# Optimization experiments

Hardware: AMD Instinct MI355X
Metric: run time of the kernel (lower is better)

Reference implementation:

```python
import jax, jax.numpy as jnp
import numpy as np

N = 100_000      # nodes
E = 1_600_000    # edges
EL = 200_000     # labeled edge pairs
NODE_DIM, HID = 32, 256
H2, H4 = HID // 2, HID // 4  # 128, 64


def _lin(k, fan_in, fan_out):
    kw, kb = jax.random.split(k)
    bound = 1.0 / np.sqrt(fan_in)
    W = jax.random.uniform(kw, (fan_in, fan_out), jnp.float32, -bound, bound)
    b = jax.random.uniform(kb, (fan_out,), jnp.float32, -bound, bound)
    return W, b


def setup_inputs() -> dict:
    key = jax.random.key(0)
    ks = jax.random.split(key, 12)
    x = jax.random.normal(ks[0], (N, NODE_DIM), jnp.float32)
    edge_index = jax.random.randint(ks[1], (2, E), 0, N, jnp.int64)
    edge_label_index = jax.random.randint(ks[2], (2, EL), 0, N, jnp.int64)
    enc_w1, enc_b1 = _lin(ks[3], NODE_DIM, HID)
    enc_w2, enc_b2 = _lin(ks[4], HID, H2)
    conv_w0, conv_b0 = _lin(ks[5], H2, H4)
    conv_w1, conv_b1 = _lin(ks[6], H4, H4)
    conv_w2, conv_b2 = _lin(ks[7], H4, H4)
    ep_w1, ep_b1 = _lin(ks[8], 2 * H4, H2)
    ep_w2, ep_b2 = _lin(ks[9], H2, H4)
    ep_w3, ep_b3 = _lin(ks[10], H4, 1)
    return dict(x=x, edge_index=edge_index, edge_label_index=edge_label_index,
                enc_w1=enc_w1, enc_b1=enc_b1, enc_w2=enc_w2, enc_b2=enc_b2,
                conv_w0=conv_w0, conv_b0=conv_b0, conv_w1=conv_w1, conv_b1=conv_b1,
                conv_w2=conv_w2, conv_b2=conv_b2,
                ep_w1=ep_w1, ep_b1=ep_b1, ep_w2=ep_w2, ep_b2=ep_b2, ep_w3=ep_w3, ep_b3=ep_b3)


def reference(x, edge_index, edge_label_index,
              enc_w1, enc_b1, enc_w2, enc_b2,
              conv_w0, conv_b0, conv_w1, conv_b1, conv_w2, conv_b2,
              ep_w1, ep_b1, ep_w2, ep_b2, ep_w3, ep_b3):
    # node encoder (dropout = identity in eval)
    h = jax.nn.relu(x @ enc_w1 + enc_b1)
    h = jax.nn.relu(h @ enc_w2 + enc_b2)           # [N, 128]

    # GCN normalization with self-loops (PyG gcn_norm, edge_weight=1)
    loops = jnp.arange(N, dtype=edge_index.dtype)
    src = jnp.concatenate([edge_index[0], loops])   # [E+N]
    dst = jnp.concatenate([edge_index[1], loops])
    deg = jax.ops.segment_sum(jnp.ones(E + N, jnp.float32), dst, num_segments=N)
    dinv = jnp.where(deg > 0, jax.lax.rsqrt(jnp.maximum(deg, 1.0)), 0.0)
    norm = (dinv[src] * dinv[dst])[:, None]          # [E+N, 1]

    def gcn(h, W, b):
        xw = h @ W                                   # transform first (PyG)
        agg = jax.ops.segment_sum(xw[src] * norm, dst, num_segments=N)
        return agg + b

    for W, b in ((conv_w0, conv_b0), (conv_w1, conv_b1), (conv_w2, conv_b2)):
        h_new = jax.nn.relu(gcn(h, W, b))
        h = h + h_new if h.shape == h_new.shape else h_new
        # self.dropout -> identity in eval

    # edge predictor on labeled pairs
    ef = jnp.concatenate([h[edge_label_index[0]], h[edge_label_index[1]]], axis=1)  # [EL, 128]
    e = jax.nn.relu(ef @ ep_w1 + ep_b1)
    e = jax.nn.relu(e @ ep_w2 + ep_b2)
    e = jax.nn.sigmoid(e @ ep_w3 + ep_b3)
    return e.squeeze(-1)                             # [EL]
```

## Files before the change

### kernel.cpp

```cpp
#include <hip/hip_runtime.h>
#include <math.h>


#define N_NODES 100000
#define N_EDGES 1600000
#define N_EL    200000

#define KBUCK   98
#define WSHIFT  10
#define WMASK   1023
#define BCAP    128
#define BSTRIDE 24576
#define PART_NB 512
#define CHUNK   3125
#define LCAP    20480

typedef __attribute__((ext_vector_type(8))) short short8_t;
typedef __attribute__((ext_vector_type(4))) float f32x4;

__device__ __forceinline__ unsigned short f2bf(float f) {
    unsigned u = __float_as_uint(f);
    unsigned r = u + 0x7FFFu + ((u >> 16) & 1u);
    return (unsigned short)(r >> 16);
}

__device__ __forceinline__ float2 up16(unsigned u) {
    union { unsigned v; _Float16 h[2]; } c; c.v = u;
    return make_float2((float)c.h[0], (float)c.h[1]);
}

template<int KTOT, int NTOT>
__device__ __forceinline__ void wprep_one(const float* __restrict__ W, unsigned short* __restrict__ Wp, int flat) {
    if (flat >= KTOT * NTOT) return;
    int j = flat & 7, lane = (flat >> 3) & 63, kstep = (flat >> 9) & 1;
    int rest = flat >> 10;
    int ntile = rest % (NTOT / 16), chunk = rest / (NTOT / 16);
    int k = chunk * 64 + kstep * 32 + (lane >> 4) * 8 + j;
    int n = ntile * 16 + (lane & 15);
    Wp[flat] = f2bf(W[(size_t)k * NTOT + n]);
}

__device__ __forceinline__ void wprep32_one(const float* __restrict__ W, unsigned short* __restrict__ Wp, int flat) {
    if (flat >= 32 * 256) return;
    int j = flat & 7, lane = (flat >> 3) & 63, ntile = flat >> 9;
    int k = (lane >> 4) * 8 + j;
    int n = ntile * 16 + (lane & 15);
    Wp[flat] = f2bf(W[(size_t)k * 256 + n]);
}

__global__ __launch_bounds__(256) void fill_part(const int* __restrict__ ei,
                                                 int* __restrict__ btail, int* __restrict__ bscr,
    const float* w2, const float* w0, const float* w1, const float* wpp2, const float* w1e,
    const float* wc1, const float* wc2,
    unsigned short* p2, unsigned short* p0, unsigned short* p1, unsigned short* pp2,
    unsigned short* p1e, unsigned short* pc1, unsigned short* pc2)
{
    __shared__ int lbuf[KBUCK][BCAP];
    __shared__ int lcnt[KBUCK];
    __shared__ int offs[KBUCK + 1];
    __shared__ int gbase[KBUCK];
    int t = threadIdx.x;

    if (blockIdx.x >= PART_NB) {
        int blk = blockIdx.x - PART_NB;
        if      (blk < 128) wprep_one<256, 128>(w2,  p2,  blk * 256 + t);
        else if (blk < 160) wprep_one<128,  64>(w0,  p0,  (blk - 128) * 256 + t);
        else if (blk < 224) wprep_one<128, 128>(w1,  p1,  (blk - 160) * 256 + t);
        else if (blk < 256) wprep_one<128,  64>(wpp2, pp2, (blk - 224) * 256 + t);
        else if (blk < 288) wprep32_one(w1e, p1e, (blk - 256) * 256 + t);
        else if (blk < 304) wprep_one< 64,  64>(wc1, pc1, (blk - 288) * 256 + t);
        else                wprep_one< 64,  64>(wc2, pc2, (blk - 304) * 256 + t);
        return;
    }

    for (int i = t; i < KBUCK; i += 256) lcnt[i] = 0;
    __syncthreads();

    int e0   = blockIdx.x * CHUNK;
    int eend = e0 + CHUNK; if (eend > N_EDGES) eend = N_EDGES;
    for (int e = e0 + t; e < eend; e += 256) {
        int s = __builtin_nontemporal_load(ei + e);
        int d = __builtin_nontemporal_load(ei + N_EDGES + e);
        int b = d >> WSHIFT;
        int entry = ((d & WMASK) << 17) | s;
        int pos = atomicAdd(&lcnt[b], 1);
        if (pos < BCAP) lbuf[b][pos] = entry;
        else {
            int p = atomicAdd(&btail[b], 1);
            bscr[b * BSTRIDE + p] = entry;
        }
    }
    __syncthreads();

    if (t < KBUCK) {
        int c = lcnt[t]; if (c > BCAP) c = BCAP;
        lcnt[t] = c;
        gbase[t] = atomicAdd(&btail[t], c);
    }
    __syncthreads();
    if (t == 0) {
        offs[0] = 0;
        for (int b = 0; b < KBUCK; ++b) offs[b + 1] = offs[b] + lcnt[b];
    }
    __syncthreads();

    int T = offs[KBUCK];
    for (int i = t; i < T; i += 256) {
        int loB = 0, hiB = KBUCK;
        while (hiB - loB > 1) { int mid = (loB + hiB) >> 1; if (offs[mid] <= i) loB = mid; else hiB = mid; }
        int j = i - offs[loB];
        bscr[loB * BSTRIDE + gbase[loB] + j] = lbuf[loB][j];
    }
}

__global__ __launch_bounds__(1024) void fill_place(const int* __restrict__ btail,
                                                   const int* __restrict__ bscr,
                                                   int* __restrict__ row_ptr, float* __restrict__ dinv,
                                                   int* __restrict__ col) {
    __shared__ int ssm[128];
    __shared__ int lcnt[1024];
    __shared__ int lpre[1024];
    __shared__ int lbuf[LCAP];
    int b = blockIdx.x, t = threadIdx.x;

    if (t < 128) ssm[t] = (t < KBUCK) ? btail[t] : 0;
    lcnt[t] = 0;
    __syncthreads();
    for (int s = 1; s < 128; s <<= 1) {
        int a = 0;
        if (t < 128 && t >= s) a = ssm[t - s];
        __syncthreads();
        if (t < 128) ssm[t] += a;
        __syncthreads();
    }
    int segstart = (b == 0) ? 0 : ssm[b - 1];
    int n = btail[b];
    const int* src = bscr + b * BSTRIDE;
    for (int i = t; i < n; i += 1024)
        atomicAdd(&lcnt[src[i] >> 17], 1);
    __syncthreads();

    int c = lcnt[t];
    lpre[t] = c; __syncthreads();
    for (int s = 1; s < 1024; s <<= 1) {
        int a = (t >= s) ? lpre[t - s] : 0;
        __syncthreads();
        lpre[t] += a;
        __syncthreads();
    }
    int excl = lpre[t] - c;

    int v = (b << WSHIFT) + t;
    if (v < N_NODES) {
        row_ptr[v] = segstart + excl;
        dinv[v] = rsqrtf((float)(c + 1));
    }
    if (b == KBUCK - 1 && t == 0) row_ptr[N_NODES] = N_EDGES;
    lcnt[t] = excl;
    __syncthreads();

    if (n <= LCAP) {
        for (int i = t; i < n; i += 1024) {
            int e = src[i];
            int pos = atomicAdd(&lcnt[e >> 17], 1);
            lbuf[pos] = e & 0x1FFFF;
        }
        __syncthreads();
        for (int i = t; i < n; i += 1024)
            col[segstart + i] = lbuf[i];
    } else {
        for (int i = t; i < n; i += 1024) {
            int e = src[i];
            int pos = atomicAdd(&lcnt[e >> 17], 1);
            col[segstart + pos] = e & 0x1FFFF;
        }
    }
}

__global__ __launch_bounds__(256, 3) void mfma_encfull(
    const float* __restrict__ x,
    const unsigned short* __restrict__ Wp1, const float* __restrict__ b1,
    const unsigned short* __restrict__ Wp2, const float* __restrict__ b2,
    const unsigned short* __restrict__ Wp0, const float* __restrict__ dinv,
    _Float16* __restrict__ yout, int M)
{
    __shared__ __align__(16) unsigned short smem[25088];
    unsigned short (*As)[40]   = (unsigned short(*)[40])smem;
    unsigned short* Wls1       = smem + 2560;
    unsigned short (*H1)[264]  = (unsigned short(*)[264])smem;
    unsigned short (*H128)[136]= (unsigned short(*)[136])smem;
    unsigned short* Wls2       = smem + 16896;
    unsigned short* W0s        = smem + 16896;

    int t = threadIdx.x, wave = t >> 6, lane = t & 63;
    int m0 = blockIdx.x * 64;
    int cb = lane & 15, rq = lane >> 4;

    {
        int row = t >> 2, seg = t & 3;
        int gr = m0 + row;
        float4 a = make_float4(0.f, 0.f, 0.f, 0.f), b = a;
        if (gr < M) {
            a = *(const float4*)&x[(size_t)gr * 32 + seg * 8];
            b = *(const float4*)&x[(size_t)gr * 32 + seg * 8 + 4];
        }
        unsigned short tmp[8] = { f2bf(a.x), f2bf(a.y), f2bf(a.z), f2bf(a.w),
                                  f2bf(b.x), f2bf(b.y), f2bf(b.z), f2bf(b.w) };
        *(uint4*)&As[row][seg * 8] = *(uint4*)tmp;
    }
    #pragma unroll
    for (int j = 0; j < 4; ++j)
        ((uint4*)Wls1)[t + j * 256] = ((const uint4*)Wp1)[t + j * 256];
    __syncthreads();

    short8_t af1 = *(const short8_t*)&As[wave * 16 + cb][rq * 8];
    f32x4 acc[16];
    #pragma unroll
    for (int nt = 0; nt < 16; ++nt) {
        short8_t bf = *(const short8_t*)&Wls1[(nt * 64 + lane) * 8];
        acc[nt] = __builtin_amdgcn_mfma_f32_16x16x32_bf16(af1, bf, (f32x4){0.f, 0.f, 0.f, 0.f}, 0, 0, 0);
    }
    __syncthreads();

    #pragma unroll
    for (int nt = 0; nt < 16; ++nt) {
        int col = nt * 16 + cb;
        float bv = b1[col];
        #pragma unroll
        for (int r = 0; r < 4; ++r)
            H1[wave * 16 + rq * 4 + r][col] = f2bf(fmaxf(acc[nt][r] + bv, 0.f));
    }

    f32x4 acc2[8];
    #pragma unroll
    for (int nt = 0; nt < 8; ++nt) acc2[nt] = (f32x4){0.f, 0.f, 0.f, 0.f};
    for (int ch = 0; ch < 4; ++ch) {
        #pragma unroll
        for (int j = 0; j < 4; ++j)
            ((uint4*)Wls2)[t + j * 256] = ((const uint4*)(Wp2 + (size_t)ch * 8192))[t + j * 256];
        __syncthreads();
        #pragma unroll
        for (int ks = 0; ks < 2; ++ks) {
            short8_t af = *(const short8_t*)&H1[wave * 16 + cb][ch * 64 + ks * 32 + rq * 8];
            #pragma unroll
            for (int nt = 0; nt < 8; ++nt) {
                short8_t bf = *(const short8_t*)&Wls2[((nt * 2 + ks) * 64 + lane) * 8];
                acc2[nt] = __builtin_amdgcn_mfma_f32_16x16x32_bf16(af, bf, acc2[nt], 0, 0, 0);
            }
        }
        __syncthreads();
    }

    #pragma unroll
    for (int nt = 0; nt < 8; ++nt) {
        int col = nt * 16 + cb;
        float bv = b2[col];
        #pragma unroll
        for (int r = 0; r < 4; ++r)
            H128[wave * 16 + rq * 4 + r][col] = f2bf(fmaxf(acc2[nt][r] + bv, 0.f));
    }
    ((uint4*)W0s)[t]       = ((const uint4*)Wp0)[t];
    ((uint4*)W0s)[t + 256] = ((const uint4*)Wp0)[t + 256];
    __syncthreads();

    f32x4 acc3[4];
    #pragma unroll
    for (int nt = 0; nt < 4; ++nt) acc3[nt] = (f32x4){0.f, 0.f, 0.f, 0.f};
    #pragma unroll
    for (int ch = 0; ch < 2; ++ch) {
        #pragma unroll
        for (int ks = 0; ks < 2; ++ks) {
            short8_t af = *(const short8_t*)&H128[wave * 16 + cb][ch * 64 + ks * 32 + rq * 8];
            #pragma unroll
            for (int nt = 0; nt < 4; ++nt) {
                short8_t bf = *(const short8_t*)&W0s[(((ch * 4 + nt) * 2 + ks) * 64 + lane) * 8];
                acc3[nt] = __builtin_amdgcn_mfma_f32_16x16x32_bf16(af, bf, acc3[nt], 0, 0, 0);
            }
        }
    }

    #pragma unroll
    for (int nt = 0; nt < 4; ++nt) {
        int col = nt * 16 + cb;
        #pragma unroll
        for (int r = 0; r < 4; ++r) {
            int gr = m0 + wave * 16 + rq * 4 + r;
            if (gr < M) yout[(size_t)gr * 64 + col] = (_Float16)(acc3[nt][r] * dinv[gr]);
        }
    }
}

template<bool RESIDUAL>
__device__ __forceinline__ void aggcv_body(
    const uint4* __restrict__ y4, const int* __restrict__ row_ptr, const int* __restrict__ col,
    const float* __restrict__ dinv, const float* __restrict__ bias,
    const unsigned short* __restrict__ Wp,
    float* __restrict__ h,
    _Float16* __restrict__ yout)
{
    __shared__ __align__(16) unsigned short Ws[4096];
    __shared__ __align__(16) unsigned short Hs[32][72];
    __shared__ float Dv[32];

    int t = threadIdx.x;
    ((uint4*)Ws)[t]       = ((const uint4*)Wp)[t];
    ((uint4*)Ws)[t + 256] = ((const uint4*)Wp)[t + 256];

    int n  = t >> 3;
    int sl = t & 7;
    int v  = blockIdx.x * 32 + n;

    uint4 a = y4[(size_t)v * 8 + sl];
    float2 p0 = up16(a.x), p1 = up16(a.y), p2 = up16(a.z), p3 = up16(a.w);
    float s0 = p0.x, s1 = p0.y, s2 = p1.x, s3 = p1.y;
    float s4 = p2.x, s5 = p2.y, s6 = p3.x, s7 = p3.y;

    int s = row_ptr[v], e = row_ptr[v + 1];
    int i = s;
    for (; i + 3 < e; i += 4) {
        int u0 = col[i], u1 = col[i + 1], u2 = col[i + 2], u3 = col[i + 3];
        uint4 f0 = y4[(size_t)u0 * 8 + sl];
        uint4 f1 = y4[(size_t)u1 * 8 + sl];
        uint4 f2 = y4[(size_t)u2 * 8 + sl];
        uint4 f3 = y4[(size_t)u3 * 8 + sl];
        float2 g;
        g = up16(f0.x); s0 += g.x; s1 += g.y;  g = up16(f0.y); s2 += g.x; s3 += g.y;
        g = up16(f0.z); s4 += g.x; s5 += g.y;  g = up16(f0.w); s6 += g.x; s7 += g.y;
        g = up16(f1.x); s0 += g.x; s1 += g.y;  g = up16(f1.y); s2 += g.x; s3 += g.y;
        g = up16(f1.z); s4 += g.x; s5 += g.y;  g = up16(f1.w); s6 += g.x; s7 += g.y;
        g = up16(f2.x); s0 += g.x; s1 += g.y;  g = up16(f2.y); s2 += g.x; s3 += g.y;
        g = up16(f2.z); s4 += g.x; s5 += g.y;  g = up16(f2.w); s6 += g.x; s7 += g.y;
        g = up16(f3.x); s0 += g.x; s1 += g.y;  g = up16(f3.y); s2 += g.x; s3 += g.y;
        g = up16(f3.z); s4 += g.x; s5 += g.y;  g = up16(f3.w); s6 += g.x; s7 += g.y;
    }
    for (; i < e; ++i) {
        uint4 f = y4[(size_t)col[i] * 8 + sl];
        float2 g;
        g = up16(f.x); s0 += g.x; s1 += g.y;  g = up16(f.y); s2 += g.x; s3 += g.y;
        g = up16(f.z); s4 += g.x; s5 += g.y;  g = up16(f.w); s6 += g.x; s7 += g.y;
    }

    float dv = dinv[v];
    float4 ba = *(const float4*)&bias[sl * 8];
    float4 bb = *(const float4*)&bias[sl * 8 + 4];
    float v0 = fmaxf(dv * s0 + ba.x, 0.f), v1 = fmaxf(dv * s1 + ba.y, 0.f);
    float v2 = fmaxf(dv * s2 + ba.z, 0.f), v3 = fmaxf(dv * s3 + ba.w, 0.f);
    float v4 = fmaxf(dv * s4 + bb.x, 0.f), v5 = fmaxf(dv * s5 + bb.y, 0.f);
    float v6 = fmaxf(dv * s6 + bb.z, 0.f), v7 = fmaxf(dv * s7 + bb.w, 0.f);
    if (RESIDUAL) {
        float4 h0 = *(const float4*)&h[(size_t)v * 64 + sl * 8];
        float4 h1 = *(const float4*)&h[(size_t)v * 64 + sl * 8 + 4];
        v0 += h0.x; v1 += h0.y; v2 += h0.z; v3 += h0.w;
        v4 += h1.x; v5 += h1.y; v6 += h1.z; v7 += h1.w;
    }
    *(float4*)&h[(size_t)v * 64 + sl * 8]     = make_float4(v0, v1, v2, v3);
    *(float4*)&h[(size_t)v * 64 + sl * 8 + 4] = make_float4(v4, v5, v6, v7);
    union { unsigned short us[8]; uint4 u; } hb;
    hb.us[0] = f2bf(v0); hb.us[1] = f2bf(v1); hb.us[2] = f2bf(v2); hb.us[3] = f2bf(v3);
    hb.us[4] = f2bf(v4); hb.us[5] = f2bf(v5); hb.us[6] = f2bf(v6); hb.us[7] = f2bf(v7);
    *(uint4*)&Hs[n][sl * 8] = hb.u;
    if (sl == 0) Dv[n] = dv;
    __syncthreads();

    int wave = t >> 6, lane = t & 63;
    int rt   = wave & 1;
    int ct0  = (wave >> 1) * 2;
    f32x4 acc0 = (f32x4){0.f, 0.f, 0.f, 0.f}, acc1 = acc0;
    #pragma unroll
    for (int ks = 0; ks < 2; ++ks) {
        short8_t af = *(const short8_t*)&Hs[rt * 16 + (lane & 15)][ks * 32 + (lane >> 4) * 8];
        short8_t b0 = *(const short8_t*)&Ws[((ct0 * 2 + ks) * 64 + lane) * 8];
        short8_t b1 = *(const short8_t*)&Ws[(((ct0 + 1) * 2 + ks) * 64 + lane) * 8];
        acc0 = __builtin_amdgcn_mfma_f32_16x16x32_bf16(af, b0, acc0, 0, 0, 0);
        acc1 = __builtin_amdgcn_mfma_f32_16x16x32_bf16(af, b1, acc1, 0, 0, 0);
    }
    int cb = lane & 15, rq = lane >> 4;
    #pragma unroll
    for (int r = 0; r < 4; ++r) {
        int row = rt * 16 + rq * 4 + r;
        float dv2 = Dv[row];
        size_t go = (size_t)(blockIdx.x * 32 + row) * 64;
        yout[go + ct0 * 16 + cb]       = (_Float16)(acc0[r] * dv2);
        yout[go + (ct0 + 1) * 16 + cb] = (_Float16)(acc1[r] * dv2);
    }
}

__global__ __launch_bounds__(256, 6) void aggcv0_kernel(
    const uint4* y, const int* rp, const int* col, const float* dinv, const float* b,
    const unsigned short* Wp, float* h, _Float16* yout) {
    aggcv_body<false>(y, rp, col, dinv, b, Wp, h, yout);
}
__global__ __launch_bounds__(256, 6) void aggcv1_kernel(
    const uint4* y, const int* rp, const int* col, const float* dinv, const float* b,
    const unsigned short* Wp, float* h, _Float16* yout) {
    aggcv_body<true>(y, rp, col, dinv, b, Wp, h, yout);
}

__global__ __launch_bounds__(256) void agg2_kernel(
    const uint4* __restrict__ y4, const int* __restrict__ row_ptr, const int* __restrict__ col,
    const float* __restrict__ dinv, const float* __restrict__ bias,
    const float* __restrict__ hprev, uint4* __restrict__ hb4)
{
    int v  = blockIdx.x * 32 + (threadIdx.x >> 3);
    int sl = threadIdx.x & 7;
    if (v >= N_NODES) return;

    uint4 a = y4[(size_t)v * 8 + sl];
    float2 p0 = up16(a.x), p1 = up16(a.y), p2 = up16(a.z), p3 = up16(a.w);
    float s0 = p0.x, s1 = p0.y, s2 = p1.x, s3 = p1.y;
    float s4 = p2.x, s5 = p2.y, s6 = p3.x, s7 = p3.y;

    int s = row_ptr[v], e = row_ptr[v + 1];
    int i = s;
    for (; i + 3 < e; i += 4) {
        int u0 = col[i], u1 = col[i + 1], u2 = col[i + 2], u3 = col[i + 3];
        uint4 f0 = y4[(size_t)u0 * 8 + sl];
        uint4 f1 = y4[(size_t)u1 * 8 + sl];
        uint4 f2 = y4[(size_t)u2 * 8 + sl];
        uint4 f3 = y4[(size_t)u3 * 8 + sl];
        float2 g;
        g = up16(f0.x); s0 += g.x; s1 += g.y;  g = up16(f0.y); s2 += g.x; s3 += g.y;
        g = up16(f0.z); s4 += g.x; s5 += g.y;  g = up16(f0.w); s6 += g.x; s7 += g.y;
        g = up16(f1.x); s0 += g.x; s1 += g.y;  g = up16(f1.y); s2 += g.x; s3 += g.y;
        g = up16(f1.z); s4 += g.x; s5 += g.y;  g = up16(f1.w); s6 += g.x; s7 += g.y;
        g = up16(f2.x); s0 += g.x; s1 += g.y;  g = up16(f2.y); s2 += g.x; s3 += g.y;
        g = up16(f2.z); s4 += g.x; s5 += g.y;  g = up16(f2.w); s6 += g.x; s7 += g.y;
        g = up16(f3.x); s0 += g.x; s1 += g.y;  g = up16(f3.y); s2 += g.x; s3 += g.y;
        g = up16(f3.z); s4 += g.x; s5 += g.y;  g = up16(f3.w); s6 += g.x; s7 += g.y;
    }
    for (; i < e; ++i) {
        uint4 f = y4[(size_t)col[i] * 8 + sl];
        float2 g;
        g = up16(f.x); s0 += g.x; s1 += g.y;  g = up16(f.y); s2 += g.x; s3 += g.y;
        g = up16(f.z); s4 += g.x; s5 += g.y;  g = up16(f.w); s6 += g.x; s7 += g.y;
    }

    float dv = dinv[v];
    float4 ba = *(const float4*)&bias[sl * 8];
    float4 bb = *(const float4*)&bias[sl * 8 + 4];
    float v0 = fmaxf(dv * s0 + ba.x, 0.f), v1 = fmaxf(dv * s1 + ba.y, 0.f);
    float v2 = fmaxf(dv * s2 + ba.z, 0.f), v3 = fmaxf(dv * s3 + ba.w, 0.f);
    float v4 = fmaxf(dv * s4 + bb.x, 0.f), v5 = fmaxf(dv * s5 + bb.y, 0.f);
    float v6 = fmaxf(dv * s6 + bb.z, 0.f), v7 = fmaxf(dv * s7 + bb.w, 0.f);
    {
        float4 h0 = *(const float4*)&hprev[(size_t)v * 64 + sl * 8];
        float4 h1 = *(const float4*)&hprev[(size_t)v * 64 + sl * 8 + 4];
        v0 += h0.x; v1 += h0.y; v2 += h0.z; v3 += h0.w;
        v4 += h1.x; v5 += h1.y; v6 += h1.z; v7 += h1.w;
    }
    uint4 p;
    p.x = (unsigned)f2bf(v0) | ((unsigned)f2bf(v1) << 16);
    p.y = (unsigned)f2bf(v2) | ((unsigned)f2bf(v3) << 16);
    p.z = (unsigned)f2bf(v4) | ((unsigned)f2bf(v5) << 16);
    p.w = (unsigned)f2bf(v6) | ((unsigned)f2bf(v7) << 16);
    hb4[(size_t)v * 8 + sl] = p;
}

__global__ __launch_bounds__(256, 4) void mfma_ep12(
    const unsigned short* __restrict__ A, const int* __restrict__ gidx,
    const unsigned short* __restrict__ Wp1, const float* __restrict__ b1,
    const unsigned short* __restrict__ Wp2, const float* __restrict__ b2,
    const float* __restrict__ w3, const float* __restrict__ b3,
    float* __restrict__ out, int M)
{
    __shared__ __align__(16) unsigned short smem[12800];
    unsigned short (*As)[72] = (unsigned short(*)[72])smem;
    unsigned short* Wls = smem + 4608;

    int t = threadIdx.x, wave = t >> 6, lane = t & 63;
    int m0 = blockIdx.x * 64;
    int cb = lane & 15, rq = lane >> 4;

    f32x4 acc[8];
    #pragma unroll
    for (int nt = 0; nt < 8; ++nt) acc[nt] = (f32x4){0.f, 0.f, 0.f, 0.f};

    for (int ch = 0; ch < 2; ++ch) {
        #pragma unroll
        for (int j = 0; j < 2; ++j) {
            int idx = t + j * 256;
            int row = idx >> 3, seg = idx & 7;
            int gr = m0 + row;
            uint4 v = make_uint4(0u, 0u, 0u, 0u);
            if (gr < M) {
                int node = (ch == 0) ? gidx[gr] : gidx[N_EL + gr];
                v = *(const uint4*)(A + (size_t)node * 64 + seg * 8);
            }
            *(uint4*)&As[row][seg * 8] = v;
        }
        #pragma unroll
        for (int j = 0; j < 4; ++j) {
            int idx = t + j * 256;
            ((uint4*)Wls)[idx] = ((const uint4*)(Wp1 + (size_t)ch * 8192))[idx];
        }
        __syncthreads();

        #pragma unroll
        for (int ks = 0; ks < 2; ++ks) {
            short8_t af = *(const short8_t*)&As[wave * 16 + cb][ks * 32 + rq * 8];
            #pragma unroll
            for (int nt = 0; nt < 8; ++nt) {
                short8_t bf = *(const short8_t*)&Wls[((nt * 2 + ks) * 64 + lane) * 8];
                acc[nt] = __builtin_amdgcn_mfma_f32_16x16x32_bf16(af, bf, acc[nt], 0, 0, 0);
            }
        }
        __syncthreads();
    }

    unsigned short (*E1)[136] = (unsigned short(*)[136])smem;
    unsigned short* W2s = smem + 8704;
    #pragma unroll
    for (int nt = 0; nt < 8; ++nt) {
        int col = nt * 16 + cb;
        float bv = b1[col];
        #pragma unroll
        for (int r = 0; r < 4; ++r) {
            int row = wave * 16 + rq * 4 + r;
            E1[row][col] = f2bf(fmaxf(acc[nt][r] + bv, 0.f));
        }
    }
    ((uint4*)W2s)[t]       = ((const uint4*)Wp2)[t];
    ((uint4*)W2s)[t + 256] = ((const uint4*)Wp2)[t + 256];
    __syncthreads();

    f32x4 acc2[4];
    #pragma unroll
    for (int nt = 0; nt < 4; ++nt) acc2[nt] = (f32x4){0.f, 0.f, 0.f, 0.f};
    #pragma unroll
    for (int ch = 0; ch < 2; ++ch) {
        #pragma unroll
        for (int ks = 0; ks < 2; ++ks) {
            short8_t af = *(const short8_t*)&E1[wave * 16 + cb][ch * 64 + ks * 32 + rq * 8];
            #pragma unroll
            for (int nt = 0; nt < 4; ++nt) {
                short8_t bf = *(const short8_t*)&W2s[(((ch * 4 + nt) * 2 + ks) * 64 + lane) * 8];
                acc2[nt] = __builtin_amdgcn_mfma_f32_16x16x32_bf16(af, bf, acc2[nt], 0, 0, 0);
            }
        }
    }

    float s0 = 0.f, s1 = 0.f, s2 = 0.f, s3 = 0.f;
    #pragma unroll
    for (int nt = 0; nt < 4; ++nt) {
        int col = nt * 16 + cb;
        float bv = b2[col], wv = w3[col];
        s0 += fmaxf(acc2[nt][0] + bv, 0.f) * wv;
        s1 += fmaxf(acc2[nt][1] + bv, 0.f) * wv;
        s2 += fmaxf(acc2[nt][2] + bv, 0.f) * wv;
        s3 += fmaxf(acc2[nt][3] + bv, 0.f) * wv;
    }
    #pragma unroll
    for (int off = 1; off < 16; off <<= 1) {
        s0 += __shfl_xor(s0, off);
        s1 += __shfl_xor(s1, off);
        s2 += __shfl_xor(s2, off);
        s3 += __shfl_xor(s3, off);
    }
    if (cb == 0) {
        int gr = m0 + wave * 16 + rq * 4;
        if (gr + 3 < M) {
            float bb = b3[0];
            float4 o;
            o.x = 1.f / (1.f + expf(-(s0 + bb)));
            o.y = 1.f / (1.f + expf(-(s1 + bb)));
            o.z = 1.f / (1.f + expf(-(s2 + bb)));
            o.w = 1.f / (1.f + expf(-(s3 + bb)));
            *(float4*)&out[gr] = o;
        }
    }
}

extern "C" void kernel_launch(void* const* d_in, const int* in_sizes, int n_in,
                              void* d_out, int out_size, void* d_ws, size_t ws_size,
                              hipStream_t stream) {
    const float* x       = (const float*)d_in[0];
    const int*   ei      = (const int*)d_in[1];
    const int*   eli     = (const int*)d_in[2];
    const float* enc_w1  = (const float*)d_in[3];
    const float* enc_b1  = (const float*)d_in[4];
    const float* enc_w2  = (const float*)d_in[5];
    const float* enc_b2  = (const float*)d_in[6];
    const float* conv_w0 = (const float*)d_in[7];
    const float* conv_b0 = (const float*)d_in[8];
    const float* conv_w1 = (const float*)d_in[9];
    const float* conv_b1 = (const float*)d_in[10];
    const float* conv_w2 = (const float*)d_in[11];
    const float* conv_b2 = (const float*)d_in[12];
    const float* ep_w1   = (const float*)d_in[13];
    const float* ep_b1   = (const float*)d_in[14];
    const float* ep_w2   = (const float*)d_in[15];
    const float* ep_b2   = (const float*)d_in[16];
    const float* ep_w3   = (const float*)d_in[17];
    const float* ep_b3   = (const float*)d_in[18];
    float* out = (float*)d_out;

    float* fws = (float*)d_ws;
    _Float16* yb         = (_Float16*)fws;
    float* h64           = fws + 3200000;
    unsigned short* h64b = (unsigned short*)(fws + 9600000);
    int*   col     = (int*)(fws + 12800000);
    int*   row_ptr = col + 1600000;
    float* dinvp   = (float*)(row_ptr + 100032);
    unsigned short* w2p = (unsigned short*)(dinvp + 100000);
    unsigned short* w0p = w2p + 32768;
    unsigned short* w1p = w0p + 8192;
    unsigned short* wp2 = w1p + 16384;
    unsigned short* w1e = wp2 + 8192;
    unsigned short* wc1p = w1e + 8192;
    unsigned short* wc2p = wc1p + 4096;
    int*   btail   = (int*)(wc2p + 4096);
    int*   bscr    = btail + 128;

    _Float16* yb2 = (_Float16*)h64b;

    hipMemsetAsync(btail, 0, 128 * sizeof(int), stream);
    fill_part<<<PART_NB + 320, 256, 0, stream>>>(ei, btail, bscr,
        enc_w2, conv_w0, ep_w1, ep_w2, enc_w1, conv_w1, conv_w2,
        w2p, w0p, w1p, wp2, w1e, wc1p, wc2p);
    fill_place<<<KBUCK, 1024, 0, stream>>>(btail, bscr, row_ptr, dinvp, col);

    const int GBN = (N_NODES + 63) / 64;
    const int GBE = N_EL / 64;
    const int GBA = N_NODES / 32;

    mfma_encfull<<<GBN, 256, 0, stream>>>(x, w1e, enc_b1, w2p, enc_b2, w0p, dinvp, yb, N_NODES);

    aggcv0_kernel<<<GBA, 256, 0, stream>>>((const uint4*)yb, row_ptr, col, dinvp, conv_b0,
                                           wc1p, h64, yb2);
    aggcv1_kernel<<<GBA, 256, 0, stream>>>((const uint4*)yb2, row_ptr, col, dinvp, conv_b1,
                                           wc2p, h64, yb);
    agg2_kernel<<<GBA, 256, 0, stream>>>((const uint4*)yb, row_ptr, col, dinvp, conv_b2,
                                         h64, (uint4*)h64b);

    mfma_ep12<<<GBE, 256, 0, stream>>>(h64b, eli, w1p, ep_b1, wp2, ep_b2, ep_w3, ep_b3, out, N_EL);
}
```

Baseline: 295.8 us.

## Double CSR-build bucket count with smaller blocks, unroll neighbor gather by eight

The CSR construction now uses 196 destination buckets of 512 nodes each, handled by 512-thread fill_place blocks instead of 98 buckets of 1024. This spreads the placement work over more CUs with smaller shared-memory footprints. The aggregation kernels now issue eight neighbor-row gathers per iteration before accumulating, which raises memory-level parallelism at some register cost. The local-buffer and per-bucket capacities shrink along with the bucket size, so a skewed bucket is more likely to fall back to the direct-to-global path.

Measured after the change: 294.7 us. No clear change (-0.4%).

```diff
diff --git a/kernel.cpp b/kernel.cpp
--- a/kernel.cpp
+++ b/kernel.cpp
@@ -6,14 +6,14 @@
 #define N_EDGES 1600000
 #define N_EL    200000
 
-#define KBUCK   98
-#define WSHIFT  10
-#define WMASK   1023
-#define BCAP    128
-#define BSTRIDE 24576
+#define KBUCK   196
+#define WSHIFT  9
+#define WMASK   511
+#define BCAP    64
+#define BSTRIDE 12288
 #define PART_NB 512
 #define CHUNK   3125
-#define LCAP    20480
+#define LCAP    10240
 
 typedef __attribute__((ext_vector_type(8))) short short8_t;
 typedef __attribute__((ext_vector_type(4))) float f32x4;
@@ -113,36 +113,36 @@
     }
 }
 
-__global__ __launch_bounds__(1024) void fill_place(const int* __restrict__ btail,
-                                                   const int* __restrict__ bscr,
-                                                   int* __restrict__ row_ptr, float* __restrict__ dinv,
-                                                   int* __restrict__ col) {
-    __shared__ int ssm[128];
-    __shared__ int lcnt[1024];
-    __shared__ int lpre[1024];
+__global__ __launch_bounds__(512) void fill_place(const int* __restrict__ btail,
+                                                  const int* __restrict__ bscr,
+                                                  int* __restrict__ row_ptr, float* __restrict__ dinv,
+                                                  int* __restrict__ col) {
+    __shared__ int ssm[256];
+    __shared__ int lcnt[512];
+    __shared__ int lpre[512];
     __shared__ int lbuf[LCAP];
     int b = blockIdx.x, t = threadIdx.x;
 
-    if (t < 128) ssm[t] = (t < KBUCK) ? btail[t] : 0;
+    if (t < 256) ssm[t] = (t < KBUCK) ? btail[t] : 0;
     lcnt[t] = 0;
     __syncthreads();
-    for (int s = 1; s < 128; s <<= 1) {
+    for (int s = 1; s < 256; s <<= 1) {
         int a = 0;
-        if (t < 128 && t >= s) a = ssm[t - s];
-        __syncthreads();
-        if (t < 128) ssm[t] += a;
+        if (t < 256 && t >= s) a = ssm[t - s];
+        __syncthreads();
+        if (t < 256) ssm[t] += a;
         __syncthreads();
     }
     int segstart = (b == 0) ? 0 : ssm[b - 1];
     int n = btail[b];
     const int* src = bscr + b * BSTRIDE;
-    for (int i = t; i < n; i += 1024)
+    for (int i = t; i < n; i += 512)
         atomicAdd(&lcnt[src[i] >> 17], 1);
     __syncthreads();
 
     int c = lcnt[t];
     lpre[t] = c; __syncthreads();
-    for (int s = 1; s < 1024; s <<= 1) {
+    for (int s = 1; s < 512; s <<= 1) {
         int a = (t >= s) ? lpre[t - s] : 0;
         __syncthreads();
         lpre[t] += a;
@@ -160,16 +160,16 @@
     __syncthreads();
 
     if (n <= LCAP) {
-        for (int i = t; i < n; i += 1024) {
+        for (int i = t; i < n; i += 512) {
             int e = src[i];
             int pos = atomicAdd(&lcnt[e >> 17], 1);
             lbuf[pos] = e & 0x1FFFF;
         }
         __syncthreads();
-        for (int i = t; i < n; i += 1024)
+        for (int i = t; i < n; i += 512)
             col[segstart + i] = lbuf[i];
     } else {
-        for (int i = t; i < n; i += 1024) {
+        for (int i = t; i < n; i += 512) {
             int e = src[i];
             int pos = atomicAdd(&lcnt[e >> 17], 1);
             col[segstart + pos] = e & 0x1FFFF;
@@ -310,43 +310,52 @@
     int sl = t & 7;
     int v  = blockIdx.x * 32 + n;
 
-    uint4 a = y4[(size_t)v * 8 + sl];
-    float2 p0 = up16(a.x), p1 = up16(a.y), p2 = up16(a.z), p3 = up16(a.w);
-    float s0 = p0.x, s1 = p0.y, s2 = p1.x, s3 = p1.y;
-    float s4 = p2.x, s5 = p2.y, s6 = p3.x, s7 = p3.y;
-
-    int s = row_ptr[v], e = row_ptr[v + 1];
-    int i = s;
-    for (; i + 3 < e; i += 4) {
+    float s[8];
+    {
+        uint4 a = y4[(size_t)v * 8 + sl];
+        float2 g;
+        g = up16(a.x); s[0] = g.x; s[1] = g.y;  g = up16(a.y); s[2] = g.x; s[3] = g.y;
+        g = up16(a.z); s[4] = g.x; s[5] = g.y;  g = up16(a.w); s[6] = g.x; s[7] = g.y;
+    }
+    auto accrow = [&](uint4 f) {
+        float2 g;
+        g = up16(f.x); s[0] += g.x; s[1] += g.y;  g = up16(f.y); s[2] += g.x; s[3] += g.y;
+        g = up16(f.z); s[4] += g.x; s[5] += g.y;  g = up16(f.w); s[6] += g.x; s[7] += g.y;
+    };
+
+    int rs = row_ptr[v], re = row_ptr[v + 1];
+    int i = rs;
+    for (; i + 7 < re; i += 8) {
+        int u0 = col[i],     u1 = col[i + 1], u2 = col[i + 2], u3 = col[i + 3];
+        int u4 = col[i + 4], u5 = col[i + 5], u6 = col[i + 6], u7 = col[i + 7];
+        uint4 f0 = y4[(size_t)u0 * 8 + sl];
+        uint4 f1 = y4[(size_t)u1 * 8 + sl];
+        uint4 f2 = y4[(size_t)u2 * 8 + sl];
+        uint4 f3 = y4[(size_t)u3 * 8 + sl];
+        uint4 f4 = y4[(size_t)u4 * 8 + sl];
+        uint4 f5 = y4[(size_t)u5 * 8 + sl];
+        uint4 f6 = y4[(size_t)u6 * 8 + sl];
+        uint4 f7 = y4[(size_t)u7 * 8 + sl];
+        accrow(f0); accrow(f1); accrow(f2); accrow(f3);
+        accrow(f4); accrow(f5); accrow(f6); accrow(f7);
+    }
+    for (; i + 3 < re; i += 4) {
         int u0 = col[i], u1 = col[i + 1], u2 = col[i + 2], u3 = col[i + 3];
         uint4 f0 = y4[(size_t)u0 * 8 + sl];
         uint4 f1 = y4[(size_t)u1 * 8 + sl];
         uint4 f2 = y4[(size_t)u2 * 8 + sl];
         uint4 f3 = y4[(size_t)u3 * 8 + sl];
-        float2 g;
-        g = up16(f0.x); s0 += g.x; s1 += g.y;  g = up16(f0.y); s2 += g.x; s3 += g.y;
-        g = up16(f0.z); s4 += g.x; s5 += g.y;  g = up16(f0.w); s6 += g.x; s7 += g.y;
-        g = up16(f1.x); s0 += g.x; s1 += g.y;  g = up16(f1.y); s2 += g.x; s3 += g.y;
-        g = up16(f1.z); s4 += g.x; s5 += g.y;  g = up16(f1.w); s6 += g.x; s7 += g.y;
-        g = up16(f2.x); s0 += g.x; s1 += g.y;  g = up16(f2.y); s2 += g.x; s3 += g.y;
-        g = up16(f2.z); s4 += g.x; s5 += g.y;  g = up16(f2.w); s6 += g.x; s7 += g.y;
-        g = up16(f3.x); s0 += g.x; s1 += g.y;  g = up16(f3.y); s2 += g.x; s3 += g.y;
-        g = up16(f3.z); s4 += g.x; s5 += g.y;  g = up16(f3.w); s6 += g.x; s7 += g.y;
-    }
-    for (; i < e; ++i) {
-        uint4 f = y4[(size_t)col[i] * 8 + sl];
-        float2 g;
-        g = up16(f.x); s0 += g.x; s1 += g.y;  g = up16(f.y); s2 += g.x; s3 += g.y;
-        g = up16(f.z); s4 += g.x; s5 += g.y;  g = up16(f.w); s6 += g.x; s7 += g.y;
-    }
+        accrow(f0); accrow(f1); accrow(f2); accrow(f3);
+    }
+    for (; i < re; ++i) accrow(y4[(size_t)col[i] * 8 + sl]);
 
     float dv = dinv[v];
     float4 ba = *(const float4*)&bias[sl * 8];
     float4 bb = *(const float4*)&bias[sl * 8 + 4];
-    float v0 = fmaxf(dv * s0 + ba.x, 0.f), v1 = fmaxf(dv * s1 + ba.y, 0.f);
-    float v2 = fmaxf(dv * s2 + ba.z, 0.f), v3 = fmaxf(dv * s3 + ba.w, 0.f);
-    float v4 = fmaxf(dv * s4 + bb.x, 0.f), v5 = fmaxf(dv * s5 + bb.y, 0.f);
-    float v6 = fmaxf(dv * s6 + bb.z, 0.f), v7 = fmaxf(dv * s7 + bb.w, 0.f);
+    float v0 = fmaxf(dv * s[0] + ba.x, 0.f), v1 = fmaxf(dv * s[1] + ba.y, 0.f);
+    float v2 = fmaxf(dv * s[2] + ba.z, 0.f), v3 = fmaxf(dv * s[3] + ba.w, 0.f);
+    float v4 = fmaxf(dv * s[4] + bb.x, 0.f), v5 = fmaxf(dv * s[5] + bb.y, 0.f);
+    float v6 = fmaxf(dv * s[6] + bb.z, 0.f), v7 = fmaxf(dv * s[7] + bb.w, 0.f);
     if (RESIDUAL) {
         float4 h0 = *(const float4*)&h[(size_t)v * 64 + sl * 8];
         float4 h1 = *(const float4*)&h[(size_t)v * 64 + sl * 8 + 4];
@@ -405,43 +414,52 @@
     int sl = threadIdx.x & 7;
     if (v >= N_NODES) return;
 
-    uint4 a = y4[(size_t)v * 8 + sl];
-    float2 p0 = up16(a.x), p1 = up16(a.y), p2 = up16(a.z), p3 = up16(a.w);
-    float s0 = p0.x, s1 = p0.y, s2 = p1.x, s3 = p1.y;
-    float s4 = p2.x, s5 = p2.y, s6 = p3.x, s7 = p3.y;
-
-    int s = row_ptr[v], e = row_ptr[v + 1];
-    int i = s;
-    for (; i + 3 < e; i += 4) {
+    float s[8];
+    {
+        uint4 a = y4[(size_t)v * 8 + sl];
+        float2 g;
+        g = up16(a.x); s[0] = g.x; s[1] = g.y;  g = up16(a.y); s[2] = g.x; s[3] = g.y;
+        g = up16(a.z); s[4] = g.x; s[5] = g.y;  g = up16(a.w); s[6] = g.x; s[7] = g.y;
+    }
+    auto accrow = [&](uint4 f) {
+        float2 g;
+        g = up16(f.x); s[0] += g.x; s[1] += g.y;  g = up16(f.y); s[2] += g.x; s[3] += g.y;
+        g = up16(f.z); s[4] += g.x; s[5] += g.y;  g = up16(f.w); s[6] += g.x; s[7] += g.y;
+    };
+
+    int rs = row_ptr[v], re = row_ptr[v + 1];
+    int i = rs;
+    for (; i + 7 < re; i += 8) {
+        int u0 = col[i],     u1 = col[i + 1], u2 = col[i + 2], u3 = col[i + 3];
+        int u4 = col[i + 4], u5 = col[i + 5], u6 = col[i + 6], u7 = col[i + 7];
+        uint4 f0 = y4[(size_t)u0 * 8 + sl];
+        uint4 f1 = y4[(size_t)u1 * 8 + sl];
+        uint4 f2 = y4[(size_t)u2 * 8 + sl];
+        uint4 f3 = y4[(size_t)u3 * 8 + sl];
+        uint4 f4 = y4[(size_t)u4 * 8 + sl];
+        uint4 f5 = y4[(size_t)u5 * 8 + sl];
+        uint4 f6 = y4[(size_t)u6 * 8 + sl];
+        uint4 f7 = y4[(size_t)u7 * 8 + sl];
+        accrow(f0); accrow(f1); accrow(f2); accrow(f3);
+        accrow(f4); accrow(f5); accrow(f6); accrow(f7);
+    }
+    for (; i + 3 < re; i += 4) {
         int u0 = col[i], u1 = col[i + 1], u2 = col[i + 2], u3 = col[i + 3];
         uint4 f0 = y4[(size_t)u0 * 8 + sl];
         uint4 f1 = y4[(size_t)u1 * 8 + sl];
         uint4 f2 = y4[(size_t)u2 * 8 + sl];
         uint4 f3 = y4[(size_t)u3 * 8 + sl];
-        float2 g;
-        g = up16(f0.x); s0 += g.x; s1 += g.y;  g = up16(f0.y); s2 += g.x; s3 += g.y;
-        g = up16(f0.z); s4 += g.x; s5 += g.y;  g = up16(f0.w); s6 += g.x; s7 += g.y;
-        g = up16(f1.x); s0 += g.x; s1 += g.y;  g = up16(f1.y); s2 += g.x; s3 += g.y;
-        g = up16(f1.z); s4 += g.x; s5 += g.y;  g = up16(f1.w); s6 += g.x; s7 += g.y;
-        g = up16(f2.x); s0 += g.x; s1 += g.y;  g = up16(f2.y); s2 += g.x; s3 += g.y;
-        g = up16(f2.z); s4 += g.x; s5 += g.y;  g = up16(f2.w); s6 += g.x; s7 += g.y;
-        g = up16(f3.x); s0 += g.x; s1 += g.y;  g = up16(f3.y); s2 += g.x; s3 += g.y;
-        g = up16(f3.z); s4 += g.x; s5 += g.y;  g = up16(f3.w); s6 += g.x; s7 += g.y;
-    }
-    for (; i < e; ++i) {
-        uint4 f = y4[(size_t)col[i] * 8 + sl];
-        float2 g;
-        g = up16(f.x); s0 += g.x; s1 += g.y;  g = up16(f.y); s2 += g.x; s3 += g.y;
-        g = up16(f.z); s4 += g.x; s5 += g.y;  g = up16(f.w); s6 += g.x; s7 += g.y;
-    }
+        accrow(f0); accrow(f1); accrow(f2); accrow(f3);
+    }
+    for (; i < re; ++i) accrow(y4[(size_t)col[i] * 8 + sl]);
 
     float dv = dinv[v];
     float4 ba = *(const float4*)&bias[sl * 8];
     float4 bb = *(const float4*)&bias[sl * 8 + 4];
-    float v0 = fmaxf(dv * s0 + ba.x, 0.f), v1 = fmaxf(dv * s1 + ba.y, 0.f);
-    float v2 = fmaxf(dv * s2 + ba.z, 0.f), v3 = fmaxf(dv * s3 + ba.w, 0.f);
-    float v4 = fmaxf(dv * s4 + bb.x, 0.f), v5 = fmaxf(dv * s5 + bb.y, 0.f);
-    float v6 = fmaxf(dv * s6 + bb.z, 0.f), v7 = fmaxf(dv * s7 + bb.w, 0.f);
+    float v0 = fmaxf(dv * s[0] + ba.x, 0.f), v1 = fmaxf(dv * s[1] + ba.y, 0.f);
+    float v2 = fmaxf(dv * s[2] + ba.z, 0.f), v3 = fmaxf(dv * s[3] + ba.w, 0.f);
+    float v4 = fmaxf(dv * s[4] + bb.x, 0.f), v5 = fmaxf(dv * s[5] + bb.y, 0.f);
+    float v6 = fmaxf(dv * s[6] + bb.z, 0.f), v7 = fmaxf(dv * s[7] + bb.w, 0.f);
     {
         float4 h0 = *(const float4*)&hprev[(size_t)v * 64 + sl * 8];
         float4 h1 = *(const float4*)&hprev[(size_t)v * 64 + sl * 8 + 4];
@@ -609,15 +627,15 @@
     unsigned short* wc1p = w1e + 8192;
     unsigned short* wc2p = wc1p + 4096;
     int*   btail   = (int*)(wc2p + 4096);
-    int*   bscr    = btail + 128;
+    int*   bscr    = btail + 256;
 
     _Float16* yb2 = (_Float16*)h64b;
 
-    hipMemsetAsync(btail, 0, 128 * sizeof(int), stream);
+    hipMemsetAsync(btail, 0, 256 * sizeof(int), stream);
     fill_part<<<PART_NB + 320, 256, 0, stream>>>(ei, btail, bscr,
         enc_w2, conv_w0, ep_w1, ep_w2, enc_w1, conv_w1, conv_w2,
         w2p, w0p, w1p, wp2, w1e, wc1p, wc2p);
-    fill_place<<<KBUCK, 1024, 0, stream>>>(btail, bscr, row_ptr, dinvp, col);
+    fill_place<<<KBUCK, 512, 0, stream>>>(btail, bscr, row_ptr, dinvp, col);
 
     const int GBN = (N_NODES + 63) / 64;
     const int GBE = N_EL / 64;
```
